# Performance work log

Hardware: AMD Instinct MI355X
Metric: run time of the kernel (lower is better)

## Reference

```python
import jax, jax.numpy as jnp
import numpy as np

N, E = 50000, 400000
IN_DIM, OUT_DIM, EDGE_DIM, HEADS = 128, 32, 64, 8
N_REL = 512
NEG_SLOPE = 0.2  # GATv2 leaky_relu slope


def setup_inputs() -> dict:
    key = jax.random.key(0)
    ks = jax.random.split(key, 12)
    HC = HEADS * OUT_DIM
    return {
        "x": jax.random.normal(ks[0], (N, IN_DIM), jnp.float32),
        "edge_index": jax.random.randint(ks[1], (2, E), 0, N),
        "relations": jax.random.normal(ks[2], (N_REL, EDGE_DIM), jnp.float32),
        "relation_index": jax.random.randint(ks[3], (E,), 0, N_REL),
        "W_l": jax.random.normal(ks[4], (IN_DIM, HC), jnp.float32) / np.sqrt(IN_DIM),
        "b_l": jnp.zeros((HC,), jnp.float32),
        "W_r": jax.random.normal(ks[5], (IN_DIM, HC), jnp.float32) / np.sqrt(IN_DIM),
        "b_r": jnp.zeros((HC,), jnp.float32),
        "W_e": jax.random.normal(ks[6], (EDGE_DIM, HC), jnp.float32) / np.sqrt(EDGE_DIM),
        "att": jax.random.normal(ks[7], (HEADS, OUT_DIM), jnp.float32) / np.sqrt(OUT_DIM),
        "bias": jnp.zeros((OUT_DIM,), jnp.float32),
    }


def reference(x, edge_index, relations, relation_index, W_l, b_l, W_r, b_r, W_e, att, bias):
    H, C = HEADS, OUT_DIM
    src, dst = edge_index[0], edge_index[1]
    edge_attr = relations[relation_index]                       # [E, edge_dim]

    # add_self_loops with fill_value='mean': self-loop attr = mean of incoming edge_attr
    deg = jax.ops.segment_sum(jnp.ones((E,), x.dtype), dst, num_segments=N)
    attr_sum = jax.ops.segment_sum(edge_attr, dst, num_segments=N)
    self_attr = attr_sum / jnp.maximum(deg, 1.0)[:, None]        # [N, edge_dim]

    loop = jnp.arange(N)
    src_f = jnp.concatenate([src, loop])                         # [E+N]
    dst_f = jnp.concatenate([dst, loop])
    ea_f = jnp.concatenate([edge_attr, self_attr], axis=0)       # [E+N, edge_dim]

    x_l = (x @ W_l + b_l).reshape(N, H, C)
    x_r = (x @ W_r + b_r).reshape(N, H, C)
    e_emb = (ea_f @ W_e).reshape(-1, H, C)                       # [E+N, H, C]

    # GATv2 scoring: leaky_relu(x_l[src] + x_r[dst] + e_emb) . att
    m = x_l[src_f] + x_r[dst_f] + e_emb                          # [E+N, H, C]
    m = jnp.where(m >= 0, m, NEG_SLOPE * m)
    logits = jnp.einsum("ehc,hc->eh", m, att)                    # [E+N, H]

    # segment softmax over destination node
    lmax = jax.ops.segment_max(logits, dst_f, num_segments=N)    # [N, H]
    ex = jnp.exp(logits - lmax[dst_f])
    denom = jax.ops.segment_sum(ex, dst_f, num_segments=N)       # [N, H]
    alpha = ex / denom[dst_f]                                    # [E+N, H]

    # scatter-add aggregation of alpha-weighted source features
    msg = alpha[:, :, None] * x_l[src_f]                         # [E+N, H, C]
    out = jax.ops.segment_sum(msg, dst_f, num_segments=N)        # [N, H, C]
    out = out.mean(axis=1) + bias                                # concat=False -> head mean
    return (out, relations)
```

## Files before the change

### kernel.cpp

```cpp
#include <hip/hip_runtime.h>

#define N_NODES   50000
#define N_EDGES   400000
#define IN_DIM    128
#define OUT_DIM   32
#define EDGE_DIM  64
#define HEADS     8
#define HC        256
#define N_REL     512
#define NEG_SLOPE 0.2f
#define NB_SCAN   196
#define KT        64

template<int K, bool DUAL>
__global__ __launch_bounds__(256, 3) void k_gemm(
        const float* __restrict__ A,
        const float* __restrict__ W1, const float* __restrict__ b1,
        const float* __restrict__ W2, const float* __restrict__ b2,
        float* __restrict__ C1, float* __restrict__ C2, int M) {
    __shared__ float As[64][KT + 4];
    __shared__ float W1s[KT][64];
    __shared__ float W2s[DUAL ? KT : 1][64];
    const int bid = blockIdx.x;
    const int mt = bid >> 2, ct = bid & 3;
    const int n0 = mt * 64;
    const int c0 = ct * 64;
    const int t  = threadIdx.x;
    const int tx = t & 15, ty = t >> 4;

    float acc1[4][4], acc2[4][4];
    {
        float4 b14 = make_float4(0.f, 0.f, 0.f, 0.f);
        float4 b24 = make_float4(0.f, 0.f, 0.f, 0.f);
        if (b1) b14 = *(const float4*)(b1 + c0 + tx * 4);
        if (DUAL && b2) b24 = *(const float4*)(b2 + c0 + tx * 4);
#pragma unroll
        for (int mi = 0; mi < 4; ++mi) {
            acc1[mi][0] = b14.x; acc1[mi][1] = b14.y;
            acc1[mi][2] = b14.z; acc1[mi][3] = b14.w;
            acc2[mi][0] = b24.x; acc2[mi][1] = b24.y;
            acc2[mi][2] = b24.z; acc2[mi][3] = b24.w;
        }
    }

    float4 ra[4], rw1[4], rw2[4];
#pragma unroll
    for (int j = 0; j < 4; ++j) {
        const int i   = t + j * 256;
        const int row = i >> 4;
        const int cc  = (i & 15) * 4;
        ra[j] = make_float4(0.f, 0.f, 0.f, 0.f);
        if (n0 + row < M)
            ra[j] = *(const float4*)(A + (size_t)(n0 + row) * K + cc);
        rw1[j] = *(const float4*)(W1 + (size_t)row * HC + c0 + cc);
        if (DUAL)
            rw2[j] = *(const float4*)(W2 + (size_t)row * HC + c0 + cc);
    }

    for (int kt = 0; kt < K; kt += KT) {
#pragma unroll
        for (int j = 0; j < 4; ++j) {
            const int i   = t + j * 256;
            const int row = i >> 4;
            const int cc  = (i & 15) * 4;
            *(float4*)&As[row][cc]  = ra[j];
            *(float4*)&W1s[row][cc] = rw1[j];
            if (DUAL) *(float4*)&W2s[row][cc] = rw2[j];
        }
        __syncthreads();

        if (kt + KT < K) {
#pragma unroll
            for (int j = 0; j < 4; ++j) {
                const int i   = t + j * 256;
                const int row = i >> 4;
                const int cc  = (i & 15) * 4;
                ra[j] = make_float4(0.f, 0.f, 0.f, 0.f);
                if (n0 + row < M)
                    ra[j] = *(const float4*)(A + (size_t)(n0 + row) * K +
                                             kt + KT + cc);
                rw1[j] = *(const float4*)(W1 + (size_t)(kt + KT + row) * HC +
                                          c0 + cc);
                if (DUAL)
                    rw2[j] = *(const float4*)(W2 + (size_t)(kt + KT + row) * HC +
                                              c0 + cc);
            }
        }

#pragma unroll 2
        for (int k = 0; k < KT; k += 4) {
            const float4 a0 = *(const float4*)&As[ty * 4 + 0][k];
            const float4 a1 = *(const float4*)&As[ty * 4 + 1][k];
            const float4 a2 = *(const float4*)&As[ty * 4 + 2][k];
            const float4 a3 = *(const float4*)&As[ty * 4 + 3][k];
            const float4 u0 = *(const float4*)&W1s[k + 0][tx * 4];
            const float4 u1 = *(const float4*)&W1s[k + 1][tx * 4];
            const float4 u2 = *(const float4*)&W1s[k + 2][tx * 4];
            const float4 u3 = *(const float4*)&W1s[k + 3][tx * 4];
#define GSTEP(ACC, mi, AV)                                                     \
            ACC[mi][0] = fmaf(AV.x, u0.x, fmaf(AV.y, u1.x,                     \
                         fmaf(AV.z, u2.x, fmaf(AV.w, u3.x, ACC[mi][0]))));     \
            ACC[mi][1] = fmaf(AV.x, u0.y, fmaf(AV.y, u1.y,                     \
                         fmaf(AV.z, u2.y, fmaf(AV.w, u3.y, ACC[mi][1]))));     \
            ACC[mi][2] = fmaf(AV.x, u0.z, fmaf(AV.y, u1.z,                     \
                         fmaf(AV.z, u2.z, fmaf(AV.w, u3.z, ACC[mi][2]))));     \
            ACC[mi][3] = fmaf(AV.x, u0.w, fmaf(AV.y, u1.w,                     \
                         fmaf(AV.z, u2.w, fmaf(AV.w, u3.w, ACC[mi][3]))))
            GSTEP(acc1, 0, a0); GSTEP(acc1, 1, a1);
            GSTEP(acc1, 2, a2); GSTEP(acc1, 3, a3);
            if (DUAL) {
                const float4 v0 = *(const float4*)&W2s[k + 0][tx * 4];
                const float4 v1 = *(const float4*)&W2s[k + 1][tx * 4];
                const float4 v2 = *(const float4*)&W2s[k + 2][tx * 4];
                const float4 v3 = *(const float4*)&W2s[k + 3][tx * 4];
#define GSTEP2(mi, AV)                                                         \
            acc2[mi][0] = fmaf(AV.x, v0.x, fmaf(AV.y, v1.x,                    \
                          fmaf(AV.z, v2.x, fmaf(AV.w, v3.x, acc2[mi][0]))));   \
            acc2[mi][1] = fmaf(AV.x, v0.y, fmaf(AV.y, v1.y,                    \
                          fmaf(AV.z, v2.y, fmaf(AV.w, v3.y, acc2[mi][1]))));   \
            acc2[mi][2] = fmaf(AV.x, v0.z, fmaf(AV.y, v1.z,                    \
                          fmaf(AV.z, v2.z, fmaf(AV.w, v3.z, acc2[mi][2]))));   \
            acc2[mi][3] = fmaf(AV.x, v0.w, fmaf(AV.y, v1.w,                    \
                          fmaf(AV.z, v2.w, fmaf(AV.w, v3.w, acc2[mi][3]))))
                GSTEP2(0, a0); GSTEP2(1, a1); GSTEP2(2, a2); GSTEP2(3, a3);
#undef GSTEP2
            }
#undef GSTEP
        }
        __syncthreads();
    }

#pragma unroll
    for (int mi = 0; mi < 4; ++mi) {
        const int row = n0 + ty * 4 + mi;
        if (row < M) {
            float4 o1;
            o1.x = acc1[mi][0]; o1.y = acc1[mi][1];
            o1.z = acc1[mi][2]; o1.w = acc1[mi][3];
            *(float4*)(C1 + (size_t)row * HC + c0 + tx * 4) = o1;
            if (DUAL) {
                float4 o2;
                o2.x = acc2[mi][0]; o2.y = acc2[mi][1];
                o2.z = acc2[mi][2]; o2.w = acc2[mi][3];
                *(float4*)(C2 + (size_t)row * HC + c0 + tx * 4) = o2;
            }
        }
    }
}

__global__ void k_deg(const int* __restrict__ dst_arr, int* __restrict__ deg_i) {
    const int e = blockIdx.x * 256 + threadIdx.x;
    if (e < N_EDGES) atomicAdd(&deg_i[dst_arr[e]], 1);
}

__global__ void __launch_bounds__(256) k_scan_a(const int* __restrict__ deg_i,
                                                int* __restrict__ incl,
                                                int* __restrict__ partials) {
    __shared__ int s[256];
    const int i = blockIdx.x * 256 + threadIdx.x;
    const int v = (i < N_NODES) ? deg_i[i] : 0;
    s[threadIdx.x] = v;
    __syncthreads();
#pragma unroll
    for (int o = 1; o < 256; o <<= 1) {
        int t = s[threadIdx.x];
        if (threadIdx.x >= o) t += s[threadIdx.x - o];
        __syncthreads();
        s[threadIdx.x] = t;
        __syncthreads();
    }
    if (i < N_NODES) incl[i] = s[threadIdx.x];
    if (threadIdx.x == 255) partials[blockIdx.x] = s[255];
}

__global__ void __launch_bounds__(256) k_scan_b(int* __restrict__ partials) {
    __shared__ int s[256];
    const int v = (threadIdx.x < NB_SCAN) ? partials[threadIdx.x] : 0;
    s[threadIdx.x] = v;
    __syncthreads();
#pragma unroll
    for (int o = 1; o < 256; o <<= 1) {
        int t = s[threadIdx.x];
        if (threadIdx.x >= o) t += s[threadIdx.x - o];
        __syncthreads();
        s[threadIdx.x] = t;
        __syncthreads();
    }
    if (threadIdx.x < NB_SCAN) partials[threadIdx.x] = s[threadIdx.x] - v;
}

__global__ void __launch_bounds__(256) k_scan_c(const int* __restrict__ incl,
                                                const int* __restrict__ deg_i,
                                                const int* __restrict__ partials,
                                                int* __restrict__ row_ptr) {
    const int i = blockIdx.x * 256 + threadIdx.x;
    if (i < N_NODES) row_ptr[i] = incl[i] - deg_i[i] + partials[blockIdx.x];
    if (i == 0) row_ptr[N_NODES] = N_EDGES;
}

__global__ void k_fill(const int* __restrict__ src_arr,
                       const int* __restrict__ dst_arr,
                       const int* __restrict__ rel_idx,
                       const int* __restrict__ row_ptr,
                       int* __restrict__ cursor,
                       int2* __restrict__ csr) {
    const int e = blockIdx.x * 256 + threadIdx.x;
    if (e >= N_EDGES) return;
    const int d = dst_arr[e];
    const int pos = row_ptr[d] + atomicAdd(&cursor[d], 1);
    csr[pos] = make_int2(src_arr[e], rel_idx[e]);
}

__global__ void __launch_bounds__(256) k_selfattr(
        const int* __restrict__ row_ptr, const int2* __restrict__ csr,
        const float* __restrict__ relations, float* __restrict__ self_attr) {
    const int n = (blockIdx.x * 256 + threadIdx.x) >> 6;
    if (n >= N_NODES) return;
    const int lane = threadIdx.x & 63;
    const int beg = row_ptr[n], end = row_ptr[n + 1];
    float a = 0.f;
    for (int i = beg; i < end; ++i) {
        const int r = csr[i].y;
        a += relations[r * EDGE_DIM + lane];
    }
    const float dg = (float)max(end - beg, 1);
    self_attr[n * EDGE_DIM + lane] = a / dg;
}

__global__ void __launch_bounds__(256) k_agg(
        const int* __restrict__ row_ptr, const int2* __restrict__ csr,
        const float* __restrict__ x_l, const float* __restrict__ x_r,
        const float* __restrict__ rel_emb, const float* __restrict__ self_emb,
        const float* __restrict__ att, const float* __restrict__ bias,
        float* __restrict__ out) {
    const int n = (blockIdx.x * 256 + threadIdx.x) >> 6;
    if (n >= N_NODES) return;
    const int lane = threadIdx.x & 63;
    const int q = lane & 7;
    const int off = (lane >> 3) * OUT_DIM + q * 4;

    const float4 at = *(const float4*)(att + off);
    const float4 xr = *(const float4*)(x_r + (size_t)n * HC + off);

    const float4 xls = *(const float4*)(x_l + (size_t)n * HC + off);
    const float4 se  = *(const float4*)(self_emb + (size_t)n * HC + off);
    float m0 = xls.x + xr.x + se.x; m0 = m0 >= 0.f ? m0 : NEG_SLOPE * m0;
    float m1 = xls.y + xr.y + se.y; m1 = m1 >= 0.f ? m1 : NEG_SLOPE * m1;
    float m2 = xls.z + xr.z + se.z; m2 = m2 >= 0.f ? m2 : NEG_SLOPE * m2;
    float m3 = xls.w + xr.w + se.w; m3 = m3 >= 0.f ? m3 : NEG_SLOPE * m3;
    float p = at.x * m0 + at.y * m1 + at.z * m2 + at.w * m3;
    p += __shfl_xor(p, 1);
    p += __shfl_xor(p, 2);
    p += __shfl_xor(p, 4);
    float ex = __expf(p);
    float den = ex;
    float4 acc;
    acc.x = ex * xls.x; acc.y = ex * xls.y; acc.z = ex * xls.z; acc.w = ex * xls.w;

    const int beg = row_ptr[n], end = row_ptr[n + 1];
    for (int i = beg; i < end; ++i) {
        const int2 sr = csr[i];
        const float4 xl = *(const float4*)(x_l + (size_t)sr.x * HC + off);
        const float4 ev = *(const float4*)(rel_emb + (size_t)sr.y * HC + off);
        float a0 = xl.x + xr.x + ev.x; a0 = a0 >= 0.f ? a0 : NEG_SLOPE * a0;
        float a1 = xl.y + xr.y + ev.y; a1 = a1 >= 0.f ? a1 : NEG_SLOPE * a1;
        float a2 = xl.z + xr.z + ev.z; a2 = a2 >= 0.f ? a2 : NEG_SLOPE * a2;
        float a3 = xl.w + xr.w + ev.w; a3 = a3 >= 0.f ? a3 : NEG_SLOPE * a3;
        float pp = at.x * a0 + at.y * a1 + at.z * a2 + at.w * a3;
        pp += __shfl_xor(pp, 1);
        pp += __shfl_xor(pp, 2);
        pp += __shfl_xor(pp, 4);
        const float e2 = __expf(pp);
        den += e2;
        acc.x = fmaf(e2, xl.x, acc.x);
        acc.y = fmaf(e2, xl.y, acc.y);
        acc.z = fmaf(e2, xl.z, acc.z);
        acc.w = fmaf(e2, xl.w, acc.w);
    }

    const float inv = 1.f / den;
    float4 v;
    v.x = acc.x * inv; v.y = acc.y * inv; v.z = acc.z * inv; v.w = acc.w * inv;
    v.x += __shfl_xor(v.x, 8);  v.y += __shfl_xor(v.y, 8);
    v.z += __shfl_xor(v.z, 8);  v.w += __shfl_xor(v.w, 8);
    v.x += __shfl_xor(v.x, 16); v.y += __shfl_xor(v.y, 16);
    v.z += __shfl_xor(v.z, 16); v.w += __shfl_xor(v.w, 16);
    v.x += __shfl_xor(v.x, 32); v.y += __shfl_xor(v.y, 32);
    v.z += __shfl_xor(v.z, 32); v.w += __shfl_xor(v.w, 32);
    if (lane < 8) {
        const float4 bs = *(const float4*)(bias + q * 4);
        float4 o;
        o.x = v.x * 0.125f + bs.x;
        o.y = v.y * 0.125f + bs.y;
        o.z = v.z * 0.125f + bs.z;
        o.w = v.w * 0.125f + bs.w;
        *(float4*)(out + (size_t)n * OUT_DIM + q * 4) = o;
    }
}

__global__ void k_copy_rel(const float* __restrict__ relations,
                           float* __restrict__ out_tail) {
    const int i = blockIdx.x * 256 + threadIdx.x;
    if (i < N_REL * EDGE_DIM) out_tail[i] = relations[i];
}

extern "C" void kernel_launch(void* const* d_in, const int* in_sizes, int n_in,
                              void* d_out, int out_size, void* d_ws, size_t ws_size,
                              hipStream_t stream) {
    const float* x         = (const float*)d_in[0];
    const int*   edge_idx  = (const int*)d_in[1];
    const float* relations = (const float*)d_in[2];
    const int*   rel_idx   = (const int*)d_in[3];
    const float* W_l       = (const float*)d_in[4];
    const float* b_l       = (const float*)d_in[5];
    const float* W_r       = (const float*)d_in[6];
    const float* b_r       = (const float*)d_in[7];
    const float* W_e       = (const float*)d_in[8];
    const float* att       = (const float*)d_in[9];
    const float* bias      = (const float*)d_in[10];

    const int* src_arr = edge_idx;
    const int* dst_arr = edge_idx + N_EDGES;

    float* out      = (float*)d_out;
    float* out_tail = out + N_NODES * OUT_DIM;

    float* ws        = (float*)d_ws;
    float* x_l       = ws;
    float* x_r       = x_l + (size_t)N_NODES * HC;
    float* self_emb  = x_r + (size_t)N_NODES * HC;
    float* rel_emb   = self_emb + (size_t)N_NODES * HC;
    float* self_attr = rel_emb + (size_t)N_REL * HC;
    int*   ibase     = (int*)(self_attr + (size_t)N_NODES * EDGE_DIM);
    int2*  csr       = (int2*)ibase;
    int*   row_ptr   = ibase + 2 * N_EDGES;
    int*   incl      = row_ptr + N_NODES + 4;
    int*   deg_i     = incl + N_NODES;
    int*   cursor    = deg_i + N_NODES;
    int*   partials  = cursor + N_NODES;

    hipMemsetAsync(deg_i, 0, 2 * N_NODES * sizeof(int), stream);

    k_deg<<<(N_EDGES + 255) / 256, 256, 0, stream>>>(dst_arr, deg_i);
    k_scan_a<<<NB_SCAN, 256, 0, stream>>>(deg_i, incl, partials);
    k_scan_b<<<1, 256, 0, stream>>>(partials);
    k_scan_c<<<NB_SCAN, 256, 0, stream>>>(incl, deg_i, partials, row_ptr);
    k_fill<<<(N_EDGES + 255) / 256, 256, 0, stream>>>(
        src_arr, dst_arr, rel_idx, row_ptr, cursor, csr);

    const int mt_nodes = (N_NODES + 63) / 64;
    const int mt_rel   = (N_REL + 63) / 64;
    k_gemm<128, true><<<mt_nodes * 4, 256, 0, stream>>>(
        x, W_l, b_l, W_r, b_r, x_l, x_r, N_NODES);
    k_gemm<64, false><<<mt_rel * 4, 256, 0, stream>>>(
        relations, W_e, nullptr, nullptr, nullptr, rel_emb, nullptr, N_REL);

    k_selfattr<<<(N_NODES * 64 + 255) / 256, 256, 0, stream>>>(
        row_ptr, csr, relations, self_attr);
    k_gemm<64, false><<<mt_nodes * 4, 256, 0, stream>>>(
        self_attr, W_e, nullptr, nullptr, nullptr, self_emb, nullptr, N_NODES);

    k_agg<<<(N_NODES * 64 + 255) / 256, 256, 0, stream>>>(
        row_ptr, csr, x_l, x_r, rel_emb, self_emb, att, bias, out);

    k_copy_rel<<<(N_REL * EDGE_DIM + 255) / 256, 256, 0, stream>>>(
        relations, out_tail);
}
```

Measured before the change: 400.8 us.

## Loop over column tiles inside each GEMM block and pad weight shared tiles

Each GEMM block now covers a 64-row slice across all four 64-column tiles in an inner loop, instead of launching one block per row/column tile pair. This cuts the grid size by four and keeps the A rows L2-resident across column tiles. The register prefetch that overlapped global loads with compute is dropped, so every K tile loads and computes serially with an extra barrier. The weight shared-memory tiles get 4 floats of padding. Fewer blocks means less parallelism to hide latency, and the A tile is reloaded from global memory for each column tile.

Result: slower. 471.7 us (+17.7%).

```diff
diff --git a/kernel.cpp b/kernel.cpp
--- a/kernel.cpp
+++ b/kernel.cpp
@@ -19,57 +19,31 @@
         const float* __restrict__ W2, const float* __restrict__ b2,
         float* __restrict__ C1, float* __restrict__ C2, int M) {
     __shared__ float As[64][KT + 4];
-    __shared__ float W1s[KT][64];
-    __shared__ float W2s[DUAL ? KT : 1][64];
-    const int bid = blockIdx.x;
-    const int mt = bid >> 2, ct = bid & 3;
-    const int n0 = mt * 64;
-    const int c0 = ct * 64;
+    __shared__ float W1s[KT][64 + 4];
+    __shared__ float W2s[DUAL ? KT : 1][64 + 4];
+    const int n0 = blockIdx.x * 64;
     const int t  = threadIdx.x;
     const int tx = t & 15, ty = t >> 4;
 
-    float acc1[4][4], acc2[4][4];
-    {
-        float4 b14 = make_float4(0.f, 0.f, 0.f, 0.f);
-        float4 b24 = make_float4(0.f, 0.f, 0.f, 0.f);
-        if (b1) b14 = *(const float4*)(b1 + c0 + tx * 4);
-        if (DUAL && b2) b24 = *(const float4*)(b2 + c0 + tx * 4);
-#pragma unroll
-        for (int mi = 0; mi < 4; ++mi) {
-            acc1[mi][0] = b14.x; acc1[mi][1] = b14.y;
-            acc1[mi][2] = b14.z; acc1[mi][3] = b14.w;
-            acc2[mi][0] = b24.x; acc2[mi][1] = b24.y;
-            acc2[mi][2] = b24.z; acc2[mi][3] = b24.w;
+    for (int ct = 0; ct < 4; ++ct) {
+        const int c0 = ct * 64;
+        float acc1[4][4], acc2[4][4];
+        {
+            float4 b14 = make_float4(0.f, 0.f, 0.f, 0.f);
+            float4 b24 = make_float4(0.f, 0.f, 0.f, 0.f);
+            if (b1) b14 = *(const float4*)(b1 + c0 + tx * 4);
+            if (DUAL && b2) b24 = *(const float4*)(b2 + c0 + tx * 4);
+#pragma unroll
+            for (int mi = 0; mi < 4; ++mi) {
+                acc1[mi][0] = b14.x; acc1[mi][1] = b14.y;
+                acc1[mi][2] = b14.z; acc1[mi][3] = b14.w;
+                acc2[mi][0] = b24.x; acc2[mi][1] = b24.y;
+                acc2[mi][2] = b24.z; acc2[mi][3] = b24.w;
+            }
         }
-    }
-
-    float4 ra[4], rw1[4], rw2[4];
-#pragma unroll
-    for (int j = 0; j < 4; ++j) {
-        const int i   = t + j * 256;
-        const int row = i >> 4;
-        const int cc  = (i & 15) * 4;
-        ra[j] = make_float4(0.f, 0.f, 0.f, 0.f);
-        if (n0 + row < M)
-            ra[j] = *(const float4*)(A + (size_t)(n0 + row) * K + cc);
-        rw1[j] = *(const float4*)(W1 + (size_t)row * HC + c0 + cc);
-        if (DUAL)
-            rw2[j] = *(const float4*)(W2 + (size_t)row * HC + c0 + cc);
-    }
-
-    for (int kt = 0; kt < K; kt += KT) {
-#pragma unroll
-        for (int j = 0; j < 4; ++j) {
-            const int i   = t + j * 256;
-            const int row = i >> 4;
-            const int cc  = (i & 15) * 4;
-            *(float4*)&As[row][cc]  = ra[j];
-            *(float4*)&W1s[row][cc] = rw1[j];
-            if (DUAL) *(float4*)&W2s[row][cc] = rw2[j];
-        }
-        __syncthreads();
-
-        if (kt + KT < K) {
+
+        for (int kt = 0; kt < K; kt += KT) {
+            float4 ra[4], rw1[4], rw2[4];
 #pragma unroll
             for (int j = 0; j < 4; ++j) {
                 const int i   = t + j * 256;
@@ -77,74 +51,82 @@
                 const int cc  = (i & 15) * 4;
                 ra[j] = make_float4(0.f, 0.f, 0.f, 0.f);
                 if (n0 + row < M)
-                    ra[j] = *(const float4*)(A + (size_t)(n0 + row) * K +
-                                             kt + KT + cc);
-                rw1[j] = *(const float4*)(W1 + (size_t)(kt + KT + row) * HC +
-                                          c0 + cc);
+                    ra[j] = *(const float4*)(A + (size_t)(n0 + row) * K + kt + cc);
+                rw1[j] = *(const float4*)(W1 + (size_t)(kt + row) * HC + c0 + cc);
                 if (DUAL)
-                    rw2[j] = *(const float4*)(W2 + (size_t)(kt + KT + row) * HC +
-                                              c0 + cc);
+                    rw2[j] = *(const float4*)(W2 + (size_t)(kt + row) * HC + c0 + cc);
+            }
+            __syncthreads();
+#pragma unroll
+            for (int j = 0; j < 4; ++j) {
+                const int i   = t + j * 256;
+                const int row = i >> 4;
+                const int cc  = (i & 15) * 4;
+                *(float4*)&As[row][cc]  = ra[j];
+                *(float4*)&W1s[row][cc] = rw1[j];
+                if (DUAL) *(float4*)&W2s[row][cc] = rw2[j];
+            }
+            __syncthreads();
+
+#pragma unroll 2
+            for (int k = 0; k < KT; k += 4) {
+                const float4 a0 = *(const float4*)&As[ty * 4 + 0][k];
+                const float4 a1 = *(const float4*)&As[ty * 4 + 1][k];
+                const float4 a2 = *(const float4*)&As[ty * 4 + 2][k];
+                const float4 a3 = *(const float4*)&As[ty * 4 + 3][k];
+                const float4 u0 = *(const float4*)&W1s[k + 0][tx * 4];
+                const float4 u1 = *(const float4*)&W1s[k + 1][tx * 4];
+                const float4 u2 = *(const float4*)&W1s[k + 2][tx * 4];
+                const float4 u3 = *(const float4*)&W1s[k + 3][tx * 4];
+#define GSTEP(ACC, mi, AV)                                                     \
+                ACC[mi][0] = fmaf(AV.x, u0.x, fmaf(AV.y, u1.x,                 \
+                             fmaf(AV.z, u2.x, fmaf(AV.w, u3.x, ACC[mi][0])))); \
+                ACC[mi][1] = fmaf(AV.x, u0.y, fmaf(AV.y, u1.y,                 \
+                             fmaf(AV.z, u2.y, fmaf(AV.w, u3.y, ACC[mi][1])))); \
+                ACC[mi][2] = fmaf(AV.x, u0.z, fmaf(AV.y, u1.z,                 \
+                             fmaf(AV.z, u2.z, fmaf(AV.w, u3.z, ACC[mi][2])))); \
+                ACC[mi][3] = fmaf(AV.x, u0.w, fmaf(AV.y, u1.w,                 \
+                             fmaf(AV.z, u2.w, fmaf(AV.w, u3.w, ACC[mi][3]))))
+                GSTEP(acc1, 0, a0); GSTEP(acc1, 1, a1);
+                GSTEP(acc1, 2, a2); GSTEP(acc1, 3, a3);
+                if (DUAL) {
+                    const float4 v0 = *(const float4*)&W2s[k + 0][tx * 4];
+                    const float4 v1 = *(const float4*)&W2s[k + 1][tx * 4];
+                    const float4 v2 = *(const float4*)&W2s[k + 2][tx * 4];
+                    const float4 v3 = *(const float4*)&W2s[k + 3][tx * 4];
+#define GSTEP2(mi, AV)                                                         \
+                acc2[mi][0] = fmaf(AV.x, v0.x, fmaf(AV.y, v1.x,                \
+                              fmaf(AV.z, v2.x, fmaf(AV.w, v3.x, acc2[mi][0]))));\
+                acc2[mi][1] = fmaf(AV.x, v0.y, fmaf(AV.y, v1.y,                \
+                              fmaf(AV.z, v2.y, fmaf(AV.w, v3.y, acc2[mi][1]))));\
+                acc2[mi][2] = fmaf(AV.x, v0.z, fmaf(AV.y, v1.z,                \
+                              fmaf(AV.z, v2.z, fmaf(AV.w, v3.z, acc2[mi][2]))));\
+                acc2[mi][3] = fmaf(AV.x, v0.w, fmaf(AV.y, v1.w,                \
+                              fmaf(AV.z, v2.w, fmaf(AV.w, v3.w, acc2[mi][3]))))
+                    GSTEP2(0, a0); GSTEP2(1, a1); GSTEP2(2, a2); GSTEP2(3, a3);
+#undef GSTEP2
+                }
+#undef GSTEP
             }
         }
 
-#pragma unroll 2
-        for (int k = 0; k < KT; k += 4) {
-            const float4 a0 = *(const float4*)&As[ty * 4 + 0][k];
-            const float4 a1 = *(const float4*)&As[ty * 4 + 1][k];
-            const float4 a2 = *(const float4*)&As[ty * 4 + 2][k];
-            const float4 a3 = *(const float4*)&As[ty * 4 + 3][k];
-            const float4 u0 = *(const float4*)&W1s[k + 0][tx * 4];
-            const float4 u1 = *(const float4*)&W1s[k + 1][tx * 4];
-            const float4 u2 = *(const float4*)&W1s[k + 2][tx * 4];
-            const float4 u3 = *(const float4*)&W1s[k + 3][tx * 4];
-#define GSTEP(ACC, mi, AV)                                                     \
-            ACC[mi][0] = fmaf(AV.x, u0.x, fmaf(AV.y, u1.x,                     \
-                         fmaf(AV.z, u2.x, fmaf(AV.w, u3.x, ACC[mi][0]))));     \
-            ACC[mi][1] = fmaf(AV.x, u0.y, fmaf(AV.y, u1.y,                     \
-                         fmaf(AV.z, u2.y, fmaf(AV.w, u3.y, ACC[mi][1]))));     \
-            ACC[mi][2] = fmaf(AV.x, u0.z, fmaf(AV.y, u1.z,                     \
-                         fmaf(AV.z, u2.z, fmaf(AV.w, u3.z, ACC[mi][2]))));     \
-            ACC[mi][3] = fmaf(AV.x, u0.w, fmaf(AV.y, u1.w,                     \
-                         fmaf(AV.z, u2.w, fmaf(AV.w, u3.w, ACC[mi][3]))))
-            GSTEP(acc1, 0, a0); GSTEP(acc1, 1, a1);
-            GSTEP(acc1, 2, a2); GSTEP(acc1, 3, a3);
-            if (DUAL) {
-                const float4 v0 = *(const float4*)&W2s[k + 0][tx * 4];
-                const float4 v1 = *(const float4*)&W2s[k + 1][tx * 4];
-                const float4 v2 = *(const float4*)&W2s[k + 2][tx * 4];
-                const float4 v3 = *(const float4*)&W2s[k + 3][tx * 4];
-#define GSTEP2(mi, AV)                                                         \
-            acc2[mi][0] = fmaf(AV.x, v0.x, fmaf(AV.y, v1.x,                    \
-                          fmaf(AV.z, v2.x, fmaf(AV.w, v3.x, acc2[mi][0]))));   \
-            acc2[mi][1] = fmaf(AV.x, v0.y, fmaf(AV.y, v1.y,                    \
-                          fmaf(AV.z, v2.y, fmaf(AV.w, v3.y, acc2[mi][1]))));   \
-            acc2[mi][2] = fmaf(AV.x, v0.z, fmaf(AV.y, v1.z,                    \
-                          fmaf(AV.z, v2.z, fmaf(AV.w, v3.z, acc2[mi][2]))));   \
-            acc2[mi][3] = fmaf(AV.x, v0.w, fmaf(AV.y, v1.w,                    \
-                          fmaf(AV.z, v2.w, fmaf(AV.w, v3.w, acc2[mi][3]))))
-                GSTEP2(0, a0); GSTEP2(1, a1); GSTEP2(2, a2); GSTEP2(3, a3);
-#undef GSTEP2
-            }
-#undef GSTEP
+#pragma unroll
+        for (int mi = 0; mi < 4; ++mi) {
+            const int row = n0 + ty * 4 + mi;
+            if (row < M) {
+                float4 o1;
+                o1.x = acc1[mi][0]; o1.y = acc1[mi][1];
+                o1.z = acc1[mi][2]; o1.w = acc1[mi][3];
+                *(float4*)(C1 + (size_t)row * HC + c0 + tx * 4) = o1;
+                if (DUAL) {
+                    float4 o2;
+                    o2.x = acc2[mi][0]; o2.y = acc2[mi][1];
+                    o2.z = acc2[mi][2]; o2.w = acc2[mi][3];
+                    *(float4*)(C2 + (size_t)row * HC + c0 + tx * 4) = o2;
+                }
+            }
         }
         __syncthreads();
-    }
-
-#pragma unroll
-    for (int mi = 0; mi < 4; ++mi) {
-        const int row = n0 + ty * 4 + mi;
-        if (row < M) {
-            float4 o1;
-            o1.x = acc1[mi][0]; o1.y = acc1[mi][1];
-            o1.z = acc1[mi][2]; o1.w = acc1[mi][3];
-            *(float4*)(C1 + (size_t)row * HC + c0 + tx * 4) = o1;
-            if (DUAL) {
-                float4 o2;
-                o2.x = acc2[mi][0]; o2.y = acc2[mi][1];
-                o2.z = acc2[mi][2]; o2.w = acc2[mi][3];
-                *(float4*)(C2 + (size_t)row * HC + c0 + tx * 4) = o2;
-            }
-        }
     }
 }
 
@@ -348,16 +330,16 @@
     k_fill<<<(N_EDGES + 255) / 256, 256, 0, stream>>>(
         src_arr, dst_arr, rel_idx, row_ptr, cursor, csr);
 
-    const int mt_nodes = (N_NODES + 63) / 64;
-    const int mt_rel   = (N_REL + 63) / 64;
-    k_gemm<128, true><<<mt_nodes * 4, 256, 0, stream>>>(
+    const int grid_nodes = (N_NODES + 63) / 64;
+    const int grid_rel   = (N_REL + 63) / 64;
+    k_gemm<128, true><<<grid_nodes, 256, 0, stream>>>(
         x, W_l, b_l, W_r, b_r, x_l, x_r, N_NODES);
-    k_gemm<64, false><<<mt_rel * 4, 256, 0, stream>>>(
+    k_gemm<64, false><<<grid_rel, 256, 0, stream>>>(
         relations, W_e, nullptr, nullptr, nullptr, rel_emb, nullptr, N_REL);
 
     k_selfattr<<<(N_NODES * 64 + 255) / 256, 256, 0, stream>>>(
         row_ptr, csr, relations, self_attr);
-    k_gemm<64, false><<<mt_nodes * 4, 256, 0, stream>>>(
+    k_gemm<64, false><<<grid_nodes, 256, 0, stream>>>(
         self_attr, W_e, nullptr, nullptr, nullptr, self_emb, nullptr, N_NODES);
 
     k_agg<<<(N_NODES * 64 + 255) / 256, 256, 0, stream>>>(
```
